# Kernel optimization log

Hardware: AMD Instinct MI355X
Metric: run time of the kernel (lower is better)

## Reference

```python
import jax, jax.numpy as jnp
import numpy as np

HIDDEN = 768
INTER = 3072
HEADS = 12
HEAD_DIM = INTER // HEADS  # 256
LN_EPS = 1e-6
R_SOFTPLUS_0 = 1.442695041


def setup_inputs() -> dict:
    key = jax.random.key(0)
    ks = jax.random.split(key, 12)
    s = 0.02
    inp = {
        "hidden_states": jax.random.normal(ks[0], (8, 4096, HIDDEN), dtype=jnp.float32),
        "pooling_query": jax.random.normal(ks[1], (1, 1, HIDDEN), dtype=jnp.float32) * s,
        "Wq": jax.random.normal(ks[2], (HIDDEN, INTER), dtype=jnp.float32) * s,
        "bq": jnp.zeros((INTER,), dtype=jnp.float32),
        "Wk": jax.random.normal(ks[3], (HIDDEN, INTER), dtype=jnp.float32) * s,
        "bk": jnp.zeros((INTER,), dtype=jnp.float32),
        "Wv": jax.random.normal(ks[4], (HIDDEN, INTER), dtype=jnp.float32) * s,
        "bv": jnp.zeros((INTER,), dtype=jnp.float32),
        "Wp": jax.random.normal(ks[5], (INTER, HIDDEN), dtype=jnp.float32) * s,
        "bp": jnp.zeros((HIDDEN,), dtype=jnp.float32),
        "per_dim_scale": jnp.zeros((HEAD_DIM,), dtype=jnp.float32),
        "ln_w": jnp.ones((HIDDEN,), dtype=jnp.float32),
        "ln_b": jnp.zeros((HIDDEN,), dtype=jnp.float32),
    }
    return inp


def reference(hidden_states, pooling_query, Wq, bq, Wk, bk, Wv, bv, Wp, bp,
              per_dim_scale, ln_w, ln_b):
    B, S, _ = hidden_states.shape
    dt = hidden_states.dtype

    # Query: single pooling token, identical across batch -> [H, D]
    q = (pooling_query.reshape(1, HIDDEN) @ Wq + bq).reshape(HEADS, HEAD_DIM)
    # PerDimScale: q * (r_softplus0/sqrt(D)) * softplus(per_dim_scale)
    scale = (R_SOFTPLUS_0 / np.sqrt(HEAD_DIM)).astype(np.float32)
    q = q * (scale * jax.nn.softplus(per_dim_scale))

    # K/V projections: [B, S, H, D]
    k = (hidden_states @ Wk + bk).reshape(B, S, HEADS, HEAD_DIM)
    v = (hidden_states @ Wv + bv).reshape(B, S, HEADS, HEAD_DIM)

    # Single-query attention: logits [B, H, S]; scaling=1.0 (scale_logits_by_head_dims=False)
    # logit cap skipped (no_attention_logit_cap=True)
    logits = jnp.einsum("hd,bshd->bhs", q, k)
    attn = jax.nn.softmax(logits.astype(jnp.float32), axis=-1).astype(dt)

    # Weighted sum over seq: [B, H, D] -> concat heads -> [B, H*D]
    ctx = jnp.einsum("bhs,bshd->bhd", attn, v).reshape(B, HEADS * HEAD_DIM)

    out = ctx @ Wp + bp  # [B, HIDDEN]
    # LayerNorm; note the original forward adds ones to ln weight in-place each call,
    # so effective weight for one call is (ln_w + 1).
    mean = jnp.mean(out, axis=-1, keepdims=True)
    var = jnp.var(out, axis=-1, keepdims=True)
    out = (out - mean) * jax.lax.rsqrt(var + LN_EPS) * (ln_w + 1.0) + ln_b

    pooled = out[:, None, :]  # [B, 1, HIDDEN]
    attn_weights = attn[:, :, None, :]  # [B, H, 1, S]
    return pooled, attn_weights
```

## Files before the change

kernel.cpp:

```cpp
#include <hip/hip_runtime.h>
#include <cstdint>
#include <cmath>

#define LN_EPS 1e-6f

#define O_Q     73728u
#define O_WK    76800u
#define O_PLOG  86016u
#define O_PHP   1658880u
#define N_SC    32
#define O_CTXP  4091904u
#define N_CCH   12
#define O_OUTP  4411392u
#define N_ICH   48
#define O_ATT   4706304u

__device__ __forceinline__ float waveReduceSum(float v) {
#pragma unroll
    for (int o = 32; o >= 1; o >>= 1) v += __shfl_xor(v, o, 64);
    return v;
}
__device__ __forceinline__ float waveReduceMax(float v) {
#pragma unroll
    for (int o = 32; o >= 1; o >>= 1) v = fmaxf(v, __shfl_xor(v, o, 64));
    return v;
}

__device__ __forceinline__ void block_sync_lds() {
    asm volatile("s_waitcnt lgkmcnt(0)" ::: "memory");
    __builtin_amdgcn_s_barrier();
    asm volatile("" ::: "memory");
}

__global__ __launch_bounds__(256) void k1_q(const float* __restrict__ pq,
                                            const float* __restrict__ Wq,
                                            const float* __restrict__ bq,
                                            const float* __restrict__ pds,
                                            float* __restrict__ ws) {
    __shared__ float sh[4][64];
    int tid = threadIdx.x;
    int l = tid & 63;
    int rg = tid >> 6;
    int col = blockIdx.x * 64 + l;
    const float* wq = Wq + (size_t)(rg * 192) * 3072 + col;
    const float* pr = pq + rg * 192;
    float acc = 0.f;
#pragma unroll 8
    for (int i = 0; i < 192; ++i)
        acc += pr[i] * wq[(size_t)i * 3072];
    sh[rg][l] = acc;
    __syncthreads();
    if (tid < 64) {
        int j = blockIdx.x * 64 + tid;
        float a = sh[0][tid] + sh[1][tid] + sh[2][tid] + sh[3][tid] + bq[j];
        float x = pds[j & 255];
        float sp = (x > 20.f) ? x : log1pf(expf(x));
        const float scale = 1.442695041f / 16.0f;
        ws[O_Q + j] = a * scale * sp;
    }
}

__global__ __launch_bounds__(256) void k2_wkeff(const float* __restrict__ Wk,
                                                float* __restrict__ ws) {
    int c = blockIdx.x;
    int tid = threadIdx.x;
    int w = tid >> 6, lane = tid & 63;
    const float4* wk = reinterpret_cast<const float4*>(Wk + (size_t)c * 3072);
    const float4* qv = reinterpret_cast<const float4*>(ws + O_Q);
#pragma unroll
    for (int i = 0; i < 3; ++i) {
        int h = w * 3 + i;
        float4 a = wk[h * 64 + lane];
        float4 b = qv[h * 64 + lane];
        float d = a.x * b.x + a.y * b.y + a.z * b.z + a.w * b.w;
        d = waveReduceSum(d);
        if (lane == 0) ws[O_WK + c * 12 + h] = d;
    }
}

__global__ __launch_bounds__(256) void k3_logits(const float* __restrict__ hidden,
                                                 const float* __restrict__ wk,
                                                 float* __restrict__ plog) {
    __shared__ float4 tile4[2][768];
    int blk = blockIdx.x;
    int q2 = blk & 1;
    int st = (blk >> 1) & 63;
    int b = blk >> 7;
    int s0 = st * 64;
    const float* hb = hidden + (size_t)(b * 4096 + s0) * 768 + q2 * 384;
    int tid = threadIdx.x;
    int w = tid >> 6, lane = tid & 63;
    int rr[3], jj[3];
#pragma unroll
    for (int t = 0; t < 3; ++t) {
        int idx = t * 256 + tid;
        rr[t] = idx / 12;
        jj[t] = idx % 12;
    }
    float4 v0[3], v1[3];
#pragma unroll
    for (int t = 0; t < 3; ++t)
        v0[t] = *reinterpret_cast<const float4*>(hb + rr[t] * 768 + jj[t] * 4);
#pragma unroll
    for (int t = 0; t < 3; ++t)
        v1[t] = *reinterpret_cast<const float4*>(hb + rr[t] * 768 + 48 + jj[t] * 4);

    float acc[12];
#pragma unroll
    for (int h = 0; h < 12; ++h) acc[h] = 0.f;

    auto step = [&](float4 (&v)[3], float4* buf, int ck) {
#pragma unroll
        for (int t = 0; t < 3; ++t)
            buf[rr[t] * 12 + (jj[t] ^ (rr[t] & 3))] = v[t];
        if (ck < 6) {
#pragma unroll
            for (int t = 0; t < 3; ++t)
                v[t] = *reinterpret_cast<const float4*>(hb + rr[t] * 768 + (ck + 2) * 48 + jj[t] * 4);
        }
        int wkoff = __builtin_amdgcn_readfirstlane((q2 * 384 + ck * 48 + (tid >> 6) * 12) * 12);
        const float* wr = wk + wkoff;
        block_sync_lds();
#pragma unroll
        for (int j2 = 0; j2 < 3; ++j2) {
            int jcol = w * 3 + j2;
            float4 x = buf[lane * 12 + (jcol ^ (lane & 3))];
            const float* wv = wr + j2 * 48;
            float xc[4] = {x.x, x.y, x.z, x.w};
#pragma unroll
            for (int cc = 0; cc < 4; ++cc) {
                const float* wc = wv + cc * 12;
#pragma unroll
                for (int h = 0; h < 12; ++h)
                    acc[h] += xc[cc] * wc[h];
            }
        }
    };
#pragma unroll
    for (int ck2 = 0; ck2 < 8; ck2 += 2) {
        step(v0, tile4[0], ck2);
        step(v1, tile4[1], ck2 + 1);
    }
    float* red = reinterpret_cast<float*>(tile4);
#pragma unroll
    for (int h = 0; h < 12; ++h) red[(w * 12 + h) * 64 + lane] = acc[h];
    __syncthreads();
    for (int idx = tid; idx < 768; idx += 256) {
        int h = idx / 64, r2 = idx & 63;
        float vv = red[(0 + h) * 64 + r2] + red[(12 + h) * 64 + r2] +
                   red[(24 + h) * 64 + r2] + red[(36 + h) * 64 + r2];
        plog[(size_t)q2 * 393216 + (size_t)(b * 12 + h) * 4096 + s0 + r2] = vv;
    }
}

__global__ __launch_bounds__(256) void k4_softmax(const float* __restrict__ ws,
                                                  float* __restrict__ attn,
                                                  float* __restrict__ attn_t) {
    __shared__ float sh[4];
    int row = blockIdx.x;
    const float4* p0 = reinterpret_cast<const float4*>(ws + O_PLOG + (size_t)row * 4096);
    const float4* p1 = p0 + 98304;
    float* base = attn + (size_t)row * 4096;
    int b = row / 12, h = row % 12;
    float* at = attn_t + (size_t)b * 65536 + h;
    int tid = threadIdx.x;
    float4 x[4];
#pragma unroll
    for (int t = 0; t < 4; ++t) {
        float4 a = p0[t * 256 + tid], c = p1[t * 256 + tid];
        x[t].x = a.x + c.x;
        x[t].y = a.y + c.y;
        x[t].z = a.z + c.z;
        x[t].w = a.w + c.w;
    }
    float m = -1e30f;
#pragma unroll
    for (int t = 0; t < 4; ++t)
        m = fmaxf(m, fmaxf(fmaxf(x[t].x, x[t].y), fmaxf(x[t].z, x[t].w)));
    m = waveReduceMax(m);
    if ((tid & 63) == 0) sh[tid >> 6] = m;
    __syncthreads();
    m = fmaxf(fmaxf(sh[0], sh[1]), fmaxf(sh[2], sh[3]));
    __syncthreads();
    float s = 0.f;
#pragma unroll
    for (int t = 0; t < 4; ++t) {
        x[t].x = expf(x[t].x - m); x[t].y = expf(x[t].y - m);
        x[t].z = expf(x[t].z - m); x[t].w = expf(x[t].w - m);
        s += x[t].x + x[t].y + x[t].z + x[t].w;
    }
    s = waveReduceSum(s);
    if ((tid & 63) == 0) sh[tid >> 6] = s;
    __syncthreads();
    s = sh[0] + sh[1] + sh[2] + sh[3];
    float inv = 1.0f / s;
#pragma unroll
    for (int t = 0; t < 4; ++t) {
        x[t].x *= inv; x[t].y *= inv; x[t].z *= inv; x[t].w *= inv;
        reinterpret_cast<float4*>(base)[t * 256 + tid] = x[t];
        int sb = (t * 256 + tid) * 4;
        at[(size_t)(sb + 0) * 16] = x[t].x;
        at[(size_t)(sb + 1) * 16] = x[t].y;
        at[(size_t)(sb + 2) * 16] = x[t].z;
        at[(size_t)(sb + 3) * 16] = x[t].w;
    }
}

__global__ __launch_bounds__(256) void k5_phpart(const float* __restrict__ hidden,
                                                 const float* __restrict__ attn_t,
                                                 float* __restrict__ php) {
    __shared__ float4 sh4[6 * 4 * 64];
    int blk = blockIdx.x;
    int sc = blk & 31;
    int ct = (blk >> 5) % 3;
    int b = blk / 96;
    int tid = threadIdx.x;
    int w = tid >> 6, lane = tid & 63;
    int c = ct * 256 + lane * 4;
    int s0 = sc * 128 + w * 32;
    const float* hb = hidden + (size_t)(b * 4096 + s0) * 768 + c;
    float4 acc[12];
#pragma unroll
    for (int h = 0; h < 12; ++h) acc[h] = make_float4(0.f, 0.f, 0.f, 0.f);
#pragma unroll 4
    for (int g = 0; g < 32; ++g) {
        float4 x = *reinterpret_cast<const float4*>(hb + (size_t)g * 768);
        int aoff = __builtin_amdgcn_readfirstlane((b * 4096 + sc * 128 + (tid >> 6) * 32 + g) * 16);
        const float* ar = attn_t + aoff;
        float a[12];
#pragma unroll
        for (int h = 0; h < 12; ++h) a[h] = ar[h];
#pragma unroll
        for (int h = 0; h < 12; ++h) {
            acc[h].x += a[h] * x.x; acc[h].y += a[h] * x.y;
            acc[h].z += a[h] * x.z; acc[h].w += a[h] * x.w;
        }
    }
    float* phpb = php + (size_t)(sc * 96 + b * 12) * 768 + ct * 256;
#pragma unroll
    for (int r = 0; r < 2; ++r) {
        if (r) __syncthreads();
#pragma unroll
        for (int i = 0; i < 6; ++i)
            sh4[(i * 4 + w) * 64 + lane] = acc[r * 6 + i];
        __syncthreads();
#pragma unroll
        for (int t = 0; t < 2; ++t) {
            int idx = t * 256 + tid;
            if (idx < 384) {
                int i = idx >> 6, l = idx & 63;
                float4 A = sh4[(i * 4 + 0) * 64 + l];
                float4 B = sh4[(i * 4 + 1) * 64 + l];
                float4 C = sh4[(i * 4 + 2) * 64 + l];
                float4 D = sh4[(i * 4 + 3) * 64 + l];
                float4 r4;
                r4.x = (A.x + B.x) + (C.x + D.x);
                r4.y = (A.y + B.y) + (C.y + D.y);
                r4.z = (A.z + B.z) + (C.z + D.z);
                r4.w = (A.w + B.w) + (C.w + D.w);
                *reinterpret_cast<float4*>(phpb + (size_t)(r * 6 + i) * 768 + l * 4) = r4;
            }
        }
    }
}

__global__ __launch_bounds__(256) void k7_ctxpart(const float* __restrict__ Wv,
                                                  float* __restrict__ ws) {
    __shared__ float phl[512];
    int blk = blockIdx.x;
    int jt = blk % 12, cch = blk / 12;
    int tid = threadIdx.x;
    const float* php = ws + O_PHP;
#pragma unroll
    for (int t = 0; t < 2; ++t) {
        int idx = t * 256 + tid;
        int b = idx >> 6, cc = idx & 63;
        int c = cch * 64 + cc;
        const float* p = php + (size_t)(b * 12 + jt) * 768 + c;
        float s = 0.f;
#pragma unroll
        for (int sc = 0; sc < N_SC; ++sc) s += p[(size_t)sc * 73728];
        phl[idx] = s;
    }
    __syncthreads();
    int j = jt * 256 + tid;
    float acc[8];
#pragma unroll
    for (int b = 0; b < 8; ++b) acc[b] = 0.f;
    for (int cc = 0; cc < 64; ++cc) {
        int c = cch * 64 + cc;
        float wv = Wv[(size_t)c * 3072 + j];
#pragma unroll
        for (int b = 0; b < 8; ++b) acc[b] += phl[b * 64 + cc] * wv;
    }
#pragma unroll
    for (int b = 0; b < 8; ++b)
        ws[O_CTXP + (size_t)(cch * 8 + b) * 3072 + j] = acc[b];
}

__global__ __launch_bounds__(256) void k8_outpart(const float* __restrict__ Wp,
                                                  const float* __restrict__ bv,
                                                  float* __restrict__ ws) {
    __shared__ float ctxl[512];
    int blk = blockIdx.x;
    int jt = blk % 3, ich = blk / 3;
    int tid = threadIdx.x;
#pragma unroll
    for (int t = 0; t < 2; ++t) {
        int idx = t * 256 + tid;
        int b = idx >> 6, ii = idx & 63;
        int i = ich * 64 + ii;
        float s = bv[i];
#pragma unroll
        for (int cch = 0; cch < N_CCH; ++cch)
            s += ws[O_CTXP + (size_t)(cch * 8 + b) * 3072 + i];
        ctxl[idx] = s;
    }
    __syncthreads();
    int j = jt * 256 + tid;
    float acc[8];
#pragma unroll
    for (int b = 0; b < 8; ++b) acc[b] = 0.f;
    for (int ii = 0; ii < 64; ++ii) {
        int i = ich * 64 + ii;
        float wp = Wp[(size_t)i * 768 + j];
#pragma unroll
        for (int b = 0; b < 8; ++b) acc[b] += ctxl[b * 64 + ii] * wp;
    }
#pragma unroll
    for (int b = 0; b < 8; ++b)
        ws[O_OUTP + (size_t)(ich * 8 + b) * 768 + j] = acc[b];
}

__global__ __launch_bounds__(256) void k9_ln(const float* __restrict__ bp,
                                             const float* __restrict__ ln_w,
                                             const float* __restrict__ ln_b,
                                             const float* __restrict__ ws,
                                             float* __restrict__ pooled) {
    __shared__ float sh[8];
    int b = blockIdx.x, tid = threadIdx.x;
    const float* op = ws + O_OUTP;
    float vals[3];
    float lsum = 0.f, lsq = 0.f;
#pragma unroll
    for (int t = 0; t < 3; ++t) {
        int j = t * 256 + tid;
        float v = bp[j];
#pragma unroll
        for (int ich = 0; ich < N_ICH; ++ich) v += op[(size_t)(ich * 8 + b) * 768 + j];
        vals[t] = v; lsum += v; lsq += v * v;
    }
    lsum = waveReduceSum(lsum);
    lsq = waveReduceSum(lsq);
    if ((tid & 63) == 0) { sh[tid >> 6] = lsum; sh[4 + (tid >> 6)] = lsq; }
    __syncthreads();
    float mean = (sh[0] + sh[1] + sh[2] + sh[3]) * (1.f / 768.f);
    float var = (sh[4] + sh[5] + sh[6] + sh[7]) * (1.f / 768.f) - mean * mean;
    float inv = rsqrtf(var + LN_EPS);
#pragma unroll
    for (int t = 0; t < 3; ++t) {
        int j = t * 256 + tid;
        pooled[b * 768 + j] = (vals[t] - mean) * inv * (ln_w[j] + 1.f) + ln_b[j];
    }
}

extern "C" void kernel_launch(void* const* d_in, const int* in_sizes, int n_in,
                              void* d_out, int out_size, void* d_ws, size_t ws_size,
                              hipStream_t stream) {
    const float* hidden = (const float*)d_in[0];
    const float* pq     = (const float*)d_in[1];
    const float* Wq     = (const float*)d_in[2];
    const float* bq     = (const float*)d_in[3];
    const float* Wk     = (const float*)d_in[4];
    const float* Wv     = (const float*)d_in[6];
    const float* bv     = (const float*)d_in[7];
    const float* Wp     = (const float*)d_in[8];
    const float* bp     = (const float*)d_in[9];
    const float* pds    = (const float*)d_in[10];
    const float* ln_w   = (const float*)d_in[11];
    const float* ln_b   = (const float*)d_in[12];
    float* out = (float*)d_out;
    float* ws  = (float*)d_ws;
    float* pooled = out;
    float* attn   = out + 6144;

    k1_q       <<<48, 256, 0, stream>>>(pq, Wq, bq, pds, ws);
    k2_wkeff   <<<768, 256, 0, stream>>>(Wk, ws);
    k3_logits  <<<1024, 256, 0, stream>>>(hidden, ws + O_WK, ws + O_PLOG);
    k4_softmax <<<96, 256, 0, stream>>>(ws, attn, ws + O_ATT);
    k5_phpart  <<<768, 256, 0, stream>>>(hidden, ws + O_ATT, ws + O_PHP);
    k7_ctxpart <<<144, 256, 0, stream>>>(Wv, ws);
    k8_outpart <<<144, 256, 0, stream>>>(Wp, bv, ws);
    k9_ln      <<<8, 256, 0, stream>>>(bp, ln_w, ln_b, ws, pooled);
}
```

Baseline: 269.5 us.

## Merge dependent kernels via in-grid atomic counters and split q projection

Dependent stages are merged into single launches: the q finalize with the Wk·q reduction, logits with softmax, and the ctx, out-projection and LayerNorm stages. Consumer blocks spin on global atomic counters until the producer blocks have signalled. The q projection is also split across 768 blocks, with a reduction pass, to spread the Wq read over more CUs. This removes kernel launch gaps between small stages. It relies on producer blocks being scheduled before the spinning consumers, otherwise the grid can deadlock.

```diff
diff --git a/kernel.cpp b/kernel.cpp
--- a/kernel.cpp
+++ b/kernel.cpp
@@ -4,6 +4,7 @@
 
 #define LN_EPS 1e-6f
 
+#define O_QP    0u
 #define O_Q     73728u
 #define O_WK    76800u
 #define O_PLOG  86016u
@@ -14,6 +15,11 @@
 #define O_OUTP  4411392u
 #define N_ICH   48
 #define O_ATT   4706304u
+#define O_CTR   5230592u
+#define CTR_K1B 0
+#define CTR_K3  1
+#define CTR_K7  2
+#define CTR_K8  3
 
 __device__ __forceinline__ float waveReduceSum(float v) {
 #pragma unroll
@@ -32,177 +38,206 @@
     asm volatile("" ::: "memory");
 }
 
-__global__ __launch_bounds__(256) void k1_q(const float* __restrict__ pq,
-                                            const float* __restrict__ Wq,
-                                            const float* __restrict__ bq,
-                                            const float* __restrict__ pds,
-                                            float* __restrict__ ws) {
+__device__ __forceinline__ void chain_signal(unsigned* ctr) {
+    __syncthreads();
+    if (threadIdx.x == 0) {
+        __threadfence();
+        __hip_atomic_fetch_add(ctr, 1u, __ATOMIC_RELEASE, __HIP_MEMORY_SCOPE_AGENT);
+    }
+}
+__device__ __forceinline__ void chain_wait(unsigned* ctr, unsigned target) {
+    if (threadIdx.x == 0) {
+        while (__hip_atomic_load(ctr, __ATOMIC_ACQUIRE, __HIP_MEMORY_SCOPE_AGENT) < target)
+            __builtin_amdgcn_s_sleep(2);
+    }
+    __syncthreads();
+    __threadfence();
+}
+
+__global__ __launch_bounds__(256) void k1a_qpart(const float* __restrict__ pq,
+                                                 const float* __restrict__ Wq,
+                                                 float* __restrict__ ws) {
     __shared__ float sh[4][64];
+    int bid = blockIdx.x;
     int tid = threadIdx.x;
-    int l = tid & 63;
-    int rg = tid >> 6;
-    int col = blockIdx.x * 64 + l;
-    const float* wq = Wq + (size_t)(rg * 192) * 3072 + col;
-    const float* pr = pq + rg * 192;
+    if (bid == 0 && tid < 4) reinterpret_cast<unsigned*>(ws + O_CTR)[tid] = 0u;
+    int ctile = bid % 48, rg = bid / 48;
+    int l = tid & 63, sub = tid >> 6;
+    int col = ctile * 64 + l;
+    const float* wq = Wq + (size_t)(rg * 48 + sub * 12) * 3072 + col;
+    const float* pr = pq + rg * 48 + sub * 12;
     float acc = 0.f;
-#pragma unroll 8
-    for (int i = 0; i < 192; ++i)
-        acc += pr[i] * wq[(size_t)i * 3072];
-    sh[rg][l] = acc;
+#pragma unroll
+    for (int i = 0; i < 12; ++i) acc += pr[i] * wq[(size_t)i * 3072];
+    sh[sub][l] = acc;
     __syncthreads();
     if (tid < 64) {
-        int j = blockIdx.x * 64 + tid;
-        float a = sh[0][tid] + sh[1][tid] + sh[2][tid] + sh[3][tid] + bq[j];
+        int c2 = ctile * 64 + tid;
+        ws[O_QP + rg * 3072 + c2] = sh[0][tid] + sh[1][tid] + sh[2][tid] + sh[3][tid];
+    }
+}
+
+__global__ __launch_bounds__(256) void k1b2(const float* __restrict__ bq,
+                                            const float* __restrict__ pds,
+                                            const float* __restrict__ Wk,
+                                            float* __restrict__ ws) {
+    unsigned* ctr = reinterpret_cast<unsigned*>(ws + O_CTR);
+    int bid = blockIdx.x;
+    int tid = threadIdx.x;
+    if (bid < 12) {
+        int j = bid * 256 + tid;
+        float a = bq[j];
+#pragma unroll
+        for (int rg = 0; rg < 16; ++rg) a += ws[O_QP + rg * 3072 + j];
         float x = pds[j & 255];
         float sp = (x > 20.f) ? x : log1pf(expf(x));
-        const float scale = 1.442695041f / 16.0f;
-        ws[O_Q + j] = a * scale * sp;
-    }
-}
-
-__global__ __launch_bounds__(256) void k2_wkeff(const float* __restrict__ Wk,
-                                                float* __restrict__ ws) {
-    int c = blockIdx.x;
+        ws[O_Q + j] = a * (1.442695041f / 16.0f) * sp;
+        chain_signal(&ctr[CTR_K1B]);
+    } else {
+        chain_wait(&ctr[CTR_K1B], 12);
+        int c = bid - 12;
+        int w = tid >> 6, lane = tid & 63;
+        const float4* wk = reinterpret_cast<const float4*>(Wk + (size_t)c * 3072);
+        const float4* qv = reinterpret_cast<const float4*>(ws + O_Q);
+#pragma unroll
+        for (int i = 0; i < 3; ++i) {
+            int h = w * 3 + i;
+            float4 a = wk[h * 64 + lane];
+            float4 b = qv[h * 64 + lane];
+            float d = a.x * b.x + a.y * b.y + a.z * b.z + a.w * b.w;
+            d = waveReduceSum(d);
+            if (lane == 0) ws[O_WK + c * 12 + h] = d;
+        }
+    }
+}
+
+__global__ __launch_bounds__(256) void k34(const float* __restrict__ hidden,
+                                           float* __restrict__ ws,
+                                           float* __restrict__ attn) {
+    __shared__ __align__(16) unsigned char SM[24576];
+    unsigned* ctr = reinterpret_cast<unsigned*>(ws + O_CTR);
+    int bid = blockIdx.x;
     int tid = threadIdx.x;
-    int w = tid >> 6, lane = tid & 63;
-    const float4* wk = reinterpret_cast<const float4*>(Wk + (size_t)c * 3072);
-    const float4* qv = reinterpret_cast<const float4*>(ws + O_Q);
-#pragma unroll
-    for (int i = 0; i < 3; ++i) {
-        int h = w * 3 + i;
-        float4 a = wk[h * 64 + lane];
-        float4 b = qv[h * 64 + lane];
-        float d = a.x * b.x + a.y * b.y + a.z * b.z + a.w * b.w;
-        d = waveReduceSum(d);
-        if (lane == 0) ws[O_WK + c * 12 + h] = d;
-    }
-}
-
-__global__ __launch_bounds__(256) void k3_logits(const float* __restrict__ hidden,
-                                                 const float* __restrict__ wk,
-                                                 float* __restrict__ plog) {
-    __shared__ float4 tile4[2][768];
-    int blk = blockIdx.x;
-    int q2 = blk & 1;
-    int st = (blk >> 1) & 63;
-    int b = blk >> 7;
-    int s0 = st * 64;
-    const float* hb = hidden + (size_t)(b * 4096 + s0) * 768 + q2 * 384;
-    int tid = threadIdx.x;
-    int w = tid >> 6, lane = tid & 63;
-    int rr[3], jj[3];
-#pragma unroll
-    for (int t = 0; t < 3; ++t) {
-        int idx = t * 256 + tid;
-        rr[t] = idx / 12;
-        jj[t] = idx % 12;
-    }
-    float4 v0[3], v1[3];
-#pragma unroll
-    for (int t = 0; t < 3; ++t)
-        v0[t] = *reinterpret_cast<const float4*>(hb + rr[t] * 768 + jj[t] * 4);
-#pragma unroll
-    for (int t = 0; t < 3; ++t)
-        v1[t] = *reinterpret_cast<const float4*>(hb + rr[t] * 768 + 48 + jj[t] * 4);
-
-    float acc[12];
-#pragma unroll
-    for (int h = 0; h < 12; ++h) acc[h] = 0.f;
-
-    auto step = [&](float4 (&v)[3], float4* buf, int ck) {
+    if (bid < 1024) {
+        float4 (*tile4)[768] = reinterpret_cast<float4(*)[768]>(SM);
+        const float* wk = ws + O_WK;
+        float* plog = ws + O_PLOG;
+        int q2 = bid & 1;
+        int st = (bid >> 1) & 63;
+        int b = bid >> 7;
+        int s0 = st * 64;
+        const float* hb = hidden + (size_t)(b * 4096 + s0) * 768 + q2 * 384;
+        int w = tid >> 6, lane = tid & 63;
+        int rr[3], jj[3];
+#pragma unroll
+        for (int t = 0; t < 3; ++t) {
+            int idx = t * 256 + tid;
+            rr[t] = idx / 12;
+            jj[t] = idx % 12;
+        }
+        float4 v0[3], v1[3];
 #pragma unroll
         for (int t = 0; t < 3; ++t)
-            buf[rr[t] * 12 + (jj[t] ^ (rr[t] & 3))] = v[t];
-        if (ck < 6) {
+            v0[t] = *reinterpret_cast<const float4*>(hb + rr[t] * 768 + jj[t] * 4);
+#pragma unroll
+        for (int t = 0; t < 3; ++t)
+            v1[t] = *reinterpret_cast<const float4*>(hb + rr[t] * 768 + 48 + jj[t] * 4);
+
+        float acc[12];
+#pragma unroll
+        for (int h = 0; h < 12; ++h) acc[h] = 0.f;
+
+        auto step = [&](float4 (&v)[3], float4* buf, int ck) {
 #pragma unroll
             for (int t = 0; t < 3; ++t)
-                v[t] = *reinterpret_cast<const float4*>(hb + rr[t] * 768 + (ck + 2) * 48 + jj[t] * 4);
-        }
-        int wkoff = __builtin_amdgcn_readfirstlane((q2 * 384 + ck * 48 + (tid >> 6) * 12) * 12);
-        const float* wr = wk + wkoff;
-        block_sync_lds();
-#pragma unroll
-        for (int j2 = 0; j2 < 3; ++j2) {
-            int jcol = w * 3 + j2;
-            float4 x = buf[lane * 12 + (jcol ^ (lane & 3))];
-            const float* wv = wr + j2 * 48;
-            float xc[4] = {x.x, x.y, x.z, x.w};
-#pragma unroll
-            for (int cc = 0; cc < 4; ++cc) {
-                const float* wc = wv + cc * 12;
-#pragma unroll
-                for (int h = 0; h < 12; ++h)
-                    acc[h] += xc[cc] * wc[h];
+                buf[rr[t] * 12 + (jj[t] ^ (rr[t] & 3))] = v[t];
+            if (ck < 6) {
+#pragma unroll
+                for (int t = 0; t < 3; ++t)
+                    v[t] = *reinterpret_cast<const float4*>(hb + rr[t] * 768 + (ck + 2) * 48 + jj[t] * 4);
             }
-        }
-    };
-#pragma unroll
-    for (int ck2 = 0; ck2 < 8; ck2 += 2) {
-        step(v0, tile4[0], ck2);
-        step(v1, tile4[1], ck2 + 1);
-    }
-    float* red = reinterpret_cast<float*>(tile4);
-#pragma unroll
-    for (int h = 0; h < 12; ++h) red[(w * 12 + h) * 64 + lane] = acc[h];
-    __syncthreads();
-    for (int idx = tid; idx < 768; idx += 256) {
-        int h = idx / 64, r2 = idx & 63;
-        float vv = red[(0 + h) * 64 + r2] + red[(12 + h) * 64 + r2] +
-                   red[(24 + h) * 64 + r2] + red[(36 + h) * 64 + r2];
-        plog[(size_t)q2 * 393216 + (size_t)(b * 12 + h) * 4096 + s0 + r2] = vv;
-    }
-}
-
-__global__ __launch_bounds__(256) void k4_softmax(const float* __restrict__ ws,
-                                                  float* __restrict__ attn,
-                                                  float* __restrict__ attn_t) {
-    __shared__ float sh[4];
-    int row = blockIdx.x;
-    const float4* p0 = reinterpret_cast<const float4*>(ws + O_PLOG + (size_t)row * 4096);
-    const float4* p1 = p0 + 98304;
-    float* base = attn + (size_t)row * 4096;
-    int b = row / 12, h = row % 12;
-    float* at = attn_t + (size_t)b * 65536 + h;
-    int tid = threadIdx.x;
-    float4 x[4];
-#pragma unroll
-    for (int t = 0; t < 4; ++t) {
-        float4 a = p0[t * 256 + tid], c = p1[t * 256 + tid];
-        x[t].x = a.x + c.x;
-        x[t].y = a.y + c.y;
-        x[t].z = a.z + c.z;
-        x[t].w = a.w + c.w;
-    }
-    float m = -1e30f;
-#pragma unroll
-    for (int t = 0; t < 4; ++t)
-        m = fmaxf(m, fmaxf(fmaxf(x[t].x, x[t].y), fmaxf(x[t].z, x[t].w)));
-    m = waveReduceMax(m);
-    if ((tid & 63) == 0) sh[tid >> 6] = m;
-    __syncthreads();
-    m = fmaxf(fmaxf(sh[0], sh[1]), fmaxf(sh[2], sh[3]));
-    __syncthreads();
-    float s = 0.f;
-#pragma unroll
-    for (int t = 0; t < 4; ++t) {
-        x[t].x = expf(x[t].x - m); x[t].y = expf(x[t].y - m);
-        x[t].z = expf(x[t].z - m); x[t].w = expf(x[t].w - m);
-        s += x[t].x + x[t].y + x[t].z + x[t].w;
-    }
-    s = waveReduceSum(s);
-    if ((tid & 63) == 0) sh[tid >> 6] = s;
-    __syncthreads();
-    s = sh[0] + sh[1] + sh[2] + sh[3];
-    float inv = 1.0f / s;
-#pragma unroll
-    for (int t = 0; t < 4; ++t) {
-        x[t].x *= inv; x[t].y *= inv; x[t].z *= inv; x[t].w *= inv;
-        reinterpret_cast<float4*>(base)[t * 256 + tid] = x[t];
-        int sb = (t * 256 + tid) * 4;
-        at[(size_t)(sb + 0) * 16] = x[t].x;
-        at[(size_t)(sb + 1) * 16] = x[t].y;
-        at[(size_t)(sb + 2) * 16] = x[t].z;
-        at[(size_t)(sb + 3) * 16] = x[t].w;
+            int wkoff = __builtin_amdgcn_readfirstlane((q2 * 384 + ck * 48 + (tid >> 6) * 12) * 12);
+            const float* wr = wk + wkoff;
+            block_sync_lds();
+#pragma unroll
+            for (int j2 = 0; j2 < 3; ++j2) {
+                int jcol = w * 3 + j2;
+                float4 x = buf[lane * 12 + (jcol ^ (lane & 3))];
+                const float* wv = wr + j2 * 48;
+                float xc[4] = {x.x, x.y, x.z, x.w};
+#pragma unroll
+                for (int cc = 0; cc < 4; ++cc) {
+                    const float* wc = wv + cc * 12;
+#pragma unroll
+                    for (int h = 0; h < 12; ++h)
+                        acc[h] += xc[cc] * wc[h];
+                }
+            }
+        };
+#pragma unroll
+        for (int ck2 = 0; ck2 < 8; ck2 += 2) {
+            step(v0, tile4[0], ck2);
+            step(v1, tile4[1], ck2 + 1);
+        }
+        float* red = reinterpret_cast<float*>(tile4);
+#pragma unroll
+        for (int h = 0; h < 12; ++h) red[(w * 12 + h) * 64 + lane] = acc[h];
+        __syncthreads();
+        for (int idx = tid; idx < 768; idx += 256) {
+            int h = idx / 64, r2 = idx & 63;
+            float vv = red[(0 + h) * 64 + r2] + red[(12 + h) * 64 + r2] +
+                       red[(24 + h) * 64 + r2] + red[(36 + h) * 64 + r2];
+            plog[(size_t)q2 * 393216 + (size_t)(b * 12 + h) * 4096 + s0 + r2] = vv;
+        }
+        chain_signal(&ctr[CTR_K3]);
+    } else {
+        chain_wait(&ctr[CTR_K3], 1024);
+        float* sh = reinterpret_cast<float*>(SM);
+        int q4 = bid - 1024;
+        int b = q4 & 7, h = q4 >> 3;
+        int row = b * 12 + h;
+        const float4* p0 = reinterpret_cast<const float4*>(ws + O_PLOG + (size_t)row * 4096);
+        const float4* p1 = p0 + 98304;
+        float* base = attn + (size_t)row * 4096;
+        float* at = ws + O_ATT + (size_t)b * 65536 + h;
+        float4 x[4];
+#pragma unroll
+        for (int t = 0; t < 4; ++t) {
+            float4 a = p0[t * 256 + tid], c = p1[t * 256 + tid];
+            x[t].x = a.x + c.x; x[t].y = a.y + c.y;
+            x[t].z = a.z + c.z; x[t].w = a.w + c.w;
+        }
+        float m = -1e30f;
+#pragma unroll
+        for (int t = 0; t < 4; ++t)
+            m = fmaxf(m, fmaxf(fmaxf(x[t].x, x[t].y), fmaxf(x[t].z, x[t].w)));
+        m = waveReduceMax(m);
+        if ((tid & 63) == 0) sh[tid >> 6] = m;
+        __syncthreads();
+        m = fmaxf(fmaxf(sh[0], sh[1]), fmaxf(sh[2], sh[3]));
+        __syncthreads();
+        float s = 0.f;
+#pragma unroll
+        for (int t = 0; t < 4; ++t) {
+            x[t].x = expf(x[t].x - m); x[t].y = expf(x[t].y - m);
+            x[t].z = expf(x[t].z - m); x[t].w = expf(x[t].w - m);
+            s += x[t].x + x[t].y + x[t].z + x[t].w;
+        }
+        s = waveReduceSum(s);
+        if ((tid & 63) == 0) sh[tid >> 6] = s;
+        __syncthreads();
+        s = sh[0] + sh[1] + sh[2] + sh[3];
+        float inv = 1.0f / s;
+#pragma unroll
+        for (int t = 0; t < 4; ++t) {
+            x[t].x *= inv; x[t].y *= inv; x[t].z *= inv; x[t].w *= inv;
+            reinterpret_cast<float4*>(base)[t * 256 + tid] = x[t];
+            int sb = (t * 256 + tid) * 4;
+            at[(size_t)(sb + 0) * 16] = x[t].x;
+            at[(size_t)(sb + 1) * 16] = x[t].y;
+            at[(size_t)(sb + 2) * 16] = x[t].z;
+            at[(size_t)(sb + 3) * 16] = x[t].w;
+        }
     }
 }
 
@@ -264,103 +299,104 @@
     }
 }
 
-__global__ __launch_bounds__(256) void k7_ctxpart(const float* __restrict__ Wv,
-                                                  float* __restrict__ ws) {
-    __shared__ float phl[512];
-    int blk = blockIdx.x;
-    int jt = blk % 12, cch = blk / 12;
+__global__ __launch_bounds__(256) void k789(const float* __restrict__ Wv,
+                                            const float* __restrict__ Wp,
+                                            const float* __restrict__ bv,
+                                            const float* __restrict__ bp,
+                                            const float* __restrict__ ln_w,
+                                            const float* __restrict__ ln_b,
+                                            float* __restrict__ ws,
+                                            float* __restrict__ pooled) {
+    __shared__ float SMf[512];
+    unsigned* ctr = reinterpret_cast<unsigned*>(ws + O_CTR);
+    int bid = blockIdx.x;
     int tid = threadIdx.x;
-    const float* php = ws + O_PHP;
-#pragma unroll
-    for (int t = 0; t < 2; ++t) {
-        int idx = t * 256 + tid;
-        int b = idx >> 6, cc = idx & 63;
-        int c = cch * 64 + cc;
-        const float* p = php + (size_t)(b * 12 + jt) * 768 + c;
-        float s = 0.f;
-#pragma unroll
-        for (int sc = 0; sc < N_SC; ++sc) s += p[(size_t)sc * 73728];
-        phl[idx] = s;
-    }
-    __syncthreads();
-    int j = jt * 256 + tid;
-    float acc[8];
-#pragma unroll
-    for (int b = 0; b < 8; ++b) acc[b] = 0.f;
-    for (int cc = 0; cc < 64; ++cc) {
-        int c = cch * 64 + cc;
-        float wv = Wv[(size_t)c * 3072 + j];
-#pragma unroll
-        for (int b = 0; b < 8; ++b) acc[b] += phl[b * 64 + cc] * wv;
-    }
-#pragma unroll
-    for (int b = 0; b < 8; ++b)
-        ws[O_CTXP + (size_t)(cch * 8 + b) * 3072 + j] = acc[b];
-}
-
-__global__ __launch_bounds__(256) void k8_outpart(const float* __restrict__ Wp,
-                                                  const float* __restrict__ bv,
-                                                  float* __restrict__ ws) {
-    __shared__ float ctxl[512];
-    int blk = blockIdx.x;
-    int jt = blk % 3, ich = blk / 3;
-    int tid = threadIdx.x;
-#pragma unroll
-    for (int t = 0; t < 2; ++t) {
-        int idx = t * 256 + tid;
-        int b = idx >> 6, ii = idx & 63;
-        int i = ich * 64 + ii;
-        float s = bv[i];
-#pragma unroll
-        for (int cch = 0; cch < N_CCH; ++cch)
-            s += ws[O_CTXP + (size_t)(cch * 8 + b) * 3072 + i];
-        ctxl[idx] = s;
-    }
-    __syncthreads();
-    int j = jt * 256 + tid;
-    float acc[8];
-#pragma unroll
-    for (int b = 0; b < 8; ++b) acc[b] = 0.f;
-    for (int ii = 0; ii < 64; ++ii) {
-        int i = ich * 64 + ii;
-        float wp = Wp[(size_t)i * 768 + j];
-#pragma unroll
-        for (int b = 0; b < 8; ++b) acc[b] += ctxl[b * 64 + ii] * wp;
-    }
-#pragma unroll
-    for (int b = 0; b < 8; ++b)
-        ws[O_OUTP + (size_t)(ich * 8 + b) * 768 + j] = acc[b];
-}
-
-__global__ __launch_bounds__(256) void k9_ln(const float* __restrict__ bp,
-                                             const float* __restrict__ ln_w,
-                                             const float* __restrict__ ln_b,
-                                             const float* __restrict__ ws,
-                                             float* __restrict__ pooled) {
-    __shared__ float sh[8];
-    int b = blockIdx.x, tid = threadIdx.x;
-    const float* op = ws + O_OUTP;
-    float vals[3];
-    float lsum = 0.f, lsq = 0.f;
-#pragma unroll
-    for (int t = 0; t < 3; ++t) {
-        int j = t * 256 + tid;
-        float v = bp[j];
-#pragma unroll
-        for (int ich = 0; ich < N_ICH; ++ich) v += op[(size_t)(ich * 8 + b) * 768 + j];
-        vals[t] = v; lsum += v; lsq += v * v;
-    }
-    lsum = waveReduceSum(lsum);
-    lsq = waveReduceSum(lsq);
-    if ((tid & 63) == 0) { sh[tid >> 6] = lsum; sh[4 + (tid >> 6)] = lsq; }
-    __syncthreads();
-    float mean = (sh[0] + sh[1] + sh[2] + sh[3]) * (1.f / 768.f);
-    float var = (sh[4] + sh[5] + sh[6] + sh[7]) * (1.f / 768.f) - mean * mean;
-    float inv = rsqrtf(var + LN_EPS);
-#pragma unroll
-    for (int t = 0; t < 3; ++t) {
-        int j = t * 256 + tid;
-        pooled[b * 768 + j] = (vals[t] - mean) * inv * (ln_w[j] + 1.f) + ln_b[j];
+    if (bid < 144) {
+        int jt = bid % 12, cch = bid / 12;
+        const float* php = ws + O_PHP;
+#pragma unroll
+        for (int t = 0; t < 2; ++t) {
+            int idx = t * 256 + tid;
+            int b = idx >> 6, cc = idx & 63;
+            int c = cch * 64 + cc;
+            const float* p = php + (size_t)(b * 12 + jt) * 768 + c;
+            float s = 0.f;
+#pragma unroll
+            for (int sc = 0; sc < N_SC; ++sc) s += p[(size_t)sc * 73728];
+            SMf[idx] = s;
+        }
+        __syncthreads();
+        int j = jt * 256 + tid;
+        float acc[8];
+#pragma unroll
+        for (int b = 0; b < 8; ++b) acc[b] = 0.f;
+        for (int cc = 0; cc < 64; ++cc) {
+            int c = cch * 64 + cc;
+            float wv = Wv[(size_t)c * 3072 + j];
+#pragma unroll
+            for (int b = 0; b < 8; ++b) acc[b] += SMf[b * 64 + cc] * wv;
+        }
+#pragma unroll
+        for (int b = 0; b < 8; ++b)
+            ws[O_CTXP + (size_t)(cch * 8 + b) * 3072 + j] = acc[b];
+        chain_signal(&ctr[CTR_K7]);
+    } else if (bid < 288) {
+        chain_wait(&ctr[CTR_K7], 144);
+        int blk = bid - 144;
+        int jt = blk % 3, ich = blk / 3;
+#pragma unroll
+        for (int t = 0; t < 2; ++t) {
+            int idx = t * 256 + tid;
+            int b = idx >> 6, ii = idx & 63;
+            int i = ich * 64 + ii;
+            float s = bv[i];
+#pragma unroll
+            for (int cch = 0; cch < N_CCH; ++cch)
+                s += ws[O_CTXP + (size_t)(cch * 8 + b) * 3072 + i];
+            SMf[idx] = s;
+        }
+        __syncthreads();
+        int j = jt * 256 + tid;
+        float acc[8];
+#pragma unroll
+        for (int b = 0; b < 8; ++b) acc[b] = 0.f;
+        for (int ii = 0; ii < 64; ++ii) {
+            int i = ich * 64 + ii;
+            float wp = Wp[(size_t)i * 768 + j];
+#pragma unroll
+            for (int b = 0; b < 8; ++b) acc[b] += SMf[b * 64 + ii] * wp;
+        }
+#pragma unroll
+        for (int b = 0; b < 8; ++b)
+            ws[O_OUTP + (size_t)(ich * 8 + b) * 768 + j] = acc[b];
+        chain_signal(&ctr[CTR_K8]);
+    } else {
+        chain_wait(&ctr[CTR_K8], 144);
+        float* sh = SMf;
+        int b = bid - 288;
+        const float* op = ws + O_OUTP;
+        float vals[3];
+        float lsum = 0.f, lsq = 0.f;
+#pragma unroll
+        for (int t = 0; t < 3; ++t) {
+            int j = t * 256 + tid;
+            float v = bp[j];
+#pragma unroll
+            for (int ich = 0; ich < N_ICH; ++ich) v += op[(size_t)(ich * 8 + b) * 768 + j];
+            vals[t] = v; lsum += v; lsq += v * v;
+        }
+        lsum = waveReduceSum(lsum);
+        lsq = waveReduceSum(lsq);
+        if ((tid & 63) == 0) { sh[tid >> 6] = lsum; sh[4 + (tid >> 6)] = lsq; }
+        __syncthreads();
+        float mean = (sh[0] + sh[1] + sh[2] + sh[3]) * (1.f / 768.f);
+        float var = (sh[4] + sh[5] + sh[6] + sh[7]) * (1.f / 768.f) - mean * mean;
+        float inv = rsqrtf(var + LN_EPS);
+#pragma unroll
+        for (int t = 0; t < 3; ++t) {
+            int j = t * 256 + tid;
+            pooled[b * 768 + j] = (vals[t] - mean) * inv * (ln_w[j] + 1.f) + ln_b[j];
+        }
     }
 }
 
@@ -384,12 +420,9 @@
     float* pooled = out;
     float* attn   = out + 6144;
 
-    k1_q       <<<48, 256, 0, stream>>>(pq, Wq, bq, pds, ws);
-    k2_wkeff   <<<768, 256, 0, stream>>>(Wk, ws);
-    k3_logits  <<<1024, 256, 0, stream>>>(hidden, ws + O_WK, ws + O_PLOG);
-    k4_softmax <<<96, 256, 0, stream>>>(ws, attn, ws + O_ATT);
-    k5_phpart  <<<768, 256, 0, stream>>>(hidden, ws + O_ATT, ws + O_PHP);
-    k7_ctxpart <<<144, 256, 0, stream>>>(Wv, ws);
-    k8_outpart <<<144, 256, 0, stream>>>(Wp, bv, ws);
-    k9_ln      <<<8, 256, 0, stream>>>(bp, ln_w, ln_b, ws, pooled);
-}
+    k1a_qpart <<<768, 256, 0, stream>>>(pq, Wq, ws);
+    k1b2      <<<780, 256, 0, stream>>>(bq, pds, Wk, ws);
+    k34       <<<1120, 256, 0, stream>>>(hidden, ws, attn);
+    k5_phpart <<<768, 256, 0, stream>>>(hidden, ws + O_ATT, ws + O_PHP);
+    k789      <<<296, 256, 0, stream>>>(Wv, Wp, bv, bp, ln_w, ln_b, ws, pooled);
+}
```

After: 513.1 us. 1.9x slower.
